# Performance work log

Hardware: AMD Instinct MI355X
Metric: run time of the kernel (lower is better)

Reference implementation:

```python
import jax, jax.numpy as jnp
import numpy as np


def setup_inputs() -> dict:
    key = jax.random.key(0)
    k1, k2, k3 = jax.random.split(key, 3)
    B, S, H, E = 4, 4096, 7168, 256
    return {
        "hidden_states": jax.random.normal(k1, (B, S, H), dtype=jnp.float32),
        "gate_weight": jax.random.normal(k2, (E, H), dtype=jnp.float32) * (H ** -0.5),
        "bias": jax.random.normal(k3, (E,), dtype=jnp.float32) * 0.01,
        "n_group": 8,
        "topk_group": 4,
        "top_k": 8,
    }


def reference(hidden_states, gate_weight, bias, n_group, topk_group, top_k):
    B, S, H = hidden_states.shape
    E = gate_weight.shape[0]
    group_size = E // n_group
    x = hidden_states.reshape(-1, H)  # [T, H]
    logits = jnp.einsum("th,eh->te", x, gate_weight)  # [T, E]
    scores = jax.nn.sigmoid(logits) + bias  # [T, E]
    scores_g = scores.reshape(-1, n_group, group_size)  # [T, G, E/G]
    group_scores = scores_g.max(axis=-1)  # [T, G]
    _, sel_groups = jax.lax.top_k(group_scores, topk_group)  # [T, topk_group]
    # group mask: 1.0 for selected groups (indices are distinct, so sum of one-hots is 0/1)
    group_mask = jax.nn.one_hot(sel_groups, n_group, dtype=scores.dtype).sum(axis=1)  # [T, G]
    masked = (scores_g * group_mask[:, :, None]).reshape(-1, E)  # [T, E]
    weights, indices = jax.lax.top_k(masked, top_k)  # [T, top_k]
    weights = weights / (weights.sum(axis=-1, keepdims=True) + 1e-6)
    return weights.reshape(B, S, -1), indices.reshape(B, S, -1)
```

## Files before the change

### kernel.cpp

```cpp
#include <hip/hip_runtime.h>


#define TTOK 16384
#define EEXP 256
#define HDIM 7168
#define BM 64
#define BK 64
#define NSTEP (HDIM / BK)
#define NTHR 512
#define LDS_BYTES 81920

typedef __attribute__((ext_vector_type(4))) float f32x4;
typedef __attribute__((ext_vector_type(4))) _Float16 h4;
typedef __attribute__((ext_vector_type(8))) _Float16 h8;

__global__ __launch_bounds__(256) void convert_w_kernel(
    const float* __restrict__ W, _Float16* __restrict__ whi,
    _Float16* __restrict__ wlo) {
  int i = blockIdx.x * blockDim.x + threadIdx.x;
  f32x4 v = ((const f32x4*)W)[i];
  h4 hi, lo;
#pragma unroll
  for (int j = 0; j < 4; ++j) {
    float x = v[j];
    _Float16 h = (_Float16)x;
    hi[j] = h;
    lo[j] = (_Float16)((x - (float)h) * 2048.0f);
  }
  *(h4*)(whi + (size_t)i * 4) = hi;
  *(h4*)(wlo + (size_t)i * 4) = lo;
}

__device__ __forceinline__ int swz_idx(int r, int kchunk) {
  return r * 64 + ((kchunk ^ (r & 7)) << 3);
}

__global__ __launch_bounds__(NTHR) void gate_kernel(
    const float* __restrict__ X, const _Float16* __restrict__ Whi,
    const _Float16* __restrict__ Wlo, const float* __restrict__ bias,
    float* __restrict__ outw, float* __restrict__ outi) {
  extern __shared__ char smem[];
  _Float16* Ahi = (_Float16*)smem;
  _Float16* Alo = (_Float16*)(smem + 8192);
  _Float16* Bhi = (_Float16*)(smem + 16384);
  _Float16* Blo = (_Float16*)(smem + 49152);
  float (*scores)[EEXP + 1] = (float (*)[EEXP + 1])smem;

  const int tid = threadIdx.x;
  const int lane = tid & 63;
  const int wid = tid >> 6;
  const int wr = wid >> 2;
  const int wc = wid & 3;

  const int ar = tid >> 3;
  const int aq = tid & 7;
  const long arow_base = (long)(blockIdx.x * BM + ar) * HDIM;

  f32x4 ra0, ra1;
  h8 rbh[4], rbl[4];

  f32x4 acc1[2][4], acc2[2][4];
#pragma unroll
  for (int m = 0; m < 2; ++m)
#pragma unroll
    for (int n = 0; n < 4; ++n) {
      acc1[m][n] = (f32x4){0.f, 0.f, 0.f, 0.f};
      acc2[m][n] = (f32x4){0.f, 0.f, 0.f, 0.f};
    }

  auto LOAD = [&](int k0) {
    ra0 = *(const f32x4*)(X + arow_base + k0 + aq * 4);
    ra1 = *(const f32x4*)(X + arow_base + k0 + (aq + 8) * 4);
#pragma unroll
    for (int i = 0; i < 4; ++i) {
      int c = tid + i * 512;
      int r = c >> 3, cc = c & 7;
      const long off = (long)r * HDIM + k0 + cc * 8;
      rbh[i] = *(const h8*)(Whi + off);
      rbl[i] = *(const h8*)(Wlo + off);
    }
  };

  auto STORE = [&]() {
    h4 h0, l0, h1, l1;
#pragma unroll
    for (int j = 0; j < 4; ++j) {
      float x0 = ra0[j];
      _Float16 hh0 = (_Float16)x0;
      h0[j] = hh0;
      l0[j] = (_Float16)((x0 - (float)hh0) * 2048.0f);
      float x1 = ra1[j];
      _Float16 hh1 = (_Float16)x1;
      h1[j] = hh1;
      l1[j] = (_Float16)((x1 - (float)hh1) * 2048.0f);
    }
    {
      int e0 = ar * 64 + ((((aq >> 1)) ^ (ar & 7)) << 3) + (aq & 1) * 4;
      int q1 = aq + 8;
      int e1 = ar * 64 + ((((q1 >> 1)) ^ (ar & 7)) << 3) + (q1 & 1) * 4;
      *(h4*)(Ahi + e0) = h0;
      *(h4*)(Ahi + e1) = h1;
      *(h4*)(Alo + e0) = l0;
      *(h4*)(Alo + e1) = l1;
    }
#pragma unroll
    for (int i = 0; i < 4; ++i) {
      int c = tid + i * 512;
      int r = c >> 3, cc = c & 7;
      int e = swz_idx(r, cc);
      *(h8*)(Bhi + e) = rbh[i];
      *(h8*)(Blo + e) = rbl[i];
    }
  };

  LOAD(0);
#pragma unroll 1
  for (int kk = 0; kk < NSTEP; ++kk) {
    __syncthreads();
    STORE();
    __syncthreads();
    if (kk + 1 < NSTEP) LOAD((kk + 1) * BK);

#pragma unroll
    for (int s = 0; s < 2; ++s) {
      const int cc = ((s * 32 + (lane >> 4) * 8) >> 3);
      h8 ah[2], al[2];
#pragma unroll
      for (int m = 0; m < 2; ++m) {
        int r = wr * 32 + m * 16 + (lane & 15);
        int e = swz_idx(r, cc);
        ah[m] = *(h8*)(Ahi + e);
        al[m] = *(h8*)(Alo + e);
      }
#pragma unroll
      for (int n = 0; n < 4; ++n) {
        int r = wc * 64 + n * 16 + (lane & 15);
        int e = swz_idx(r, cc);
        h8 bh = *(h8*)(Bhi + e);
        h8 bl = *(h8*)(Blo + e);
#pragma unroll
        for (int m = 0; m < 2; ++m) {
          acc1[m][n] = __builtin_amdgcn_mfma_f32_16x16x32_f16(ah[m], bh, acc1[m][n], 0, 0, 0);
          acc2[m][n] = __builtin_amdgcn_mfma_f32_16x16x32_f16(ah[m], bl, acc2[m][n], 0, 0, 0);
          acc2[m][n] = __builtin_amdgcn_mfma_f32_16x16x32_f16(al[m], bh, acc2[m][n], 0, 0, 0);
        }
      }
    }
  }

  __syncthreads();

#pragma unroll
  for (int m = 0; m < 2; ++m)
#pragma unroll
    for (int n = 0; n < 4; ++n) {
      int e = wc * 64 + n * 16 + (lane & 15);
      float b = bias[e];
      int t0 = wr * 32 + m * 16 + (lane >> 4) * 4;
#pragma unroll
      for (int r = 0; r < 4; ++r) {
        float logit = acc1[m][n][r] + acc2[m][n][r] * (1.0f / 2048.0f);
        scores[t0 + r][e] = 1.0f / (1.0f + expf(-logit)) + b;
      }
    }
  __syncthreads();

  if ((lane & 7) == 0) {
    int t = wid * 8 + (lane >> 3);
    const float* sc = scores[t];

    float gmax[8];
#pragma unroll
    for (int g = 0; g < 8; ++g) {
      float mx = -1e30f;
      for (int j = 0; j < 32; ++j) mx = fmaxf(mx, sc[g * 32 + j]);
      gmax[g] = mx;
    }
    unsigned selmask = 0;
    for (int it = 0; it < 4; ++it) {
      float best = -1e30f;
      int bi = 0;
      for (int g = 0; g < 8; ++g)
        if (!((selmask >> g) & 1) && gmax[g] > best) {
          best = gmax[g];
          bi = g;
        }
      selmask |= 1u << bi;
    }
    float vals[8];
    int idx[8];
#pragma unroll
    for (int j = 0; j < 8; ++j) {
      vals[j] = -1e30f;
      idx[j] = 0;
    }
    for (int e = 0; e < 256; ++e) {
      float v = ((selmask >> (e >> 5)) & 1) ? sc[e] : 0.0f;
      if (v > vals[7]) {
        int p = 7;
        while (p > 0 && v > vals[p - 1]) {
          vals[p] = vals[p - 1];
          idx[p] = idx[p - 1];
          --p;
        }
        vals[p] = v;
        idx[p] = e;
      }
    }
    float ssum = 0.0f;
#pragma unroll
    for (int j = 0; j < 8; ++j) ssum += vals[j];
    float den = ssum + 1e-6f;
    long tg = (long)blockIdx.x * BM + t;
#pragma unroll
    for (int j = 0; j < 8; ++j) {
      outw[tg * 8 + j] = vals[j] / den;
      outi[tg * 8 + j] = (float)idx[j];
    }
  }
}

extern "C" void kernel_launch(void* const* d_in, const int* in_sizes, int n_in,
                              void* d_out, int out_size, void* d_ws, size_t ws_size,
                              hipStream_t stream) {
  const float* X = (const float*)d_in[0];
  const float* W = (const float*)d_in[1];
  const float* bias = (const float*)d_in[2];

  _Float16* whi = (_Float16*)d_ws;
  _Float16* wlo = whi + (size_t)EEXP * HDIM;

  float* outw = (float*)d_out;
  float* outi = outw + (size_t)TTOK * 8;

  hipFuncSetAttribute((const void*)gate_kernel,
                      hipFuncAttributeMaxDynamicSharedMemorySize, LDS_BYTES);

  convert_w_kernel<<<(EEXP * HDIM / 4) / 256, 256, 0, stream>>>(W, whi, wlo);
  gate_kernel<<<TTOK / BM, NTHR, LDS_BYTES, stream>>>(X, whi, wlo, bias, outw, outi);
}
```

Measured before the change: 314.6 us.

## Pre-pack gate weights into MFMA fragment layout and stream B from global to registers

The weight hi/lo fp16 split is now written in MFMA-fragment order, so each wave can load its B operands straight from global memory into registers. B is double-buffered across four k sub-steps, which removes the B staging through LDS. The tile changes to 32 tokens by 256 experts with 256 threads and BK=128. This cuts LDS use and synchronisation work per step and should allow more resident blocks. The trade-off is that twice as many blocks each re-read the whole packed weight from L2, raising L2/MALL traffic, and every k step now depends on global-load latency.

```diff
diff --git a/kernel.cpp b/kernel.cpp
--- a/kernel.cpp
+++ b/kernel.cpp
@@ -4,35 +4,37 @@
 #define TTOK 16384
 #define EEXP 256
 #define HDIM 7168
-#define BM 64
-#define BK 64
+#define BM 32
+#define BK 128
 #define NSTEP (HDIM / BK)
-#define NTHR 512
-#define LDS_BYTES 81920
+#define NTHR 256
+#define NKC (HDIM / 32)
+#define LDS_BYTES 33024
 
 typedef __attribute__((ext_vector_type(4))) float f32x4;
 typedef __attribute__((ext_vector_type(4))) _Float16 h4;
 typedef __attribute__((ext_vector_type(8))) _Float16 h8;
 
-__global__ __launch_bounds__(256) void convert_w_kernel(
-    const float* __restrict__ W, _Float16* __restrict__ whi,
-    _Float16* __restrict__ wlo) {
-  int i = blockIdx.x * blockDim.x + threadIdx.x;
-  f32x4 v = ((const f32x4*)W)[i];
-  h4 hi, lo;
-#pragma unroll
-  for (int j = 0; j < 4; ++j) {
-    float x = v[j];
+__global__ __launch_bounds__(64) void pack_w_kernel(const float* __restrict__ W,
+                                                    _Float16* __restrict__ whi,
+                                                    _Float16* __restrict__ wlo) {
+  const int kc = blockIdx.x;
+  const int eb = blockIdx.y;
+  const int lane = threadIdx.x;
+  const int e = eb * 16 + (lane & 15);
+  const int k0 = kc * 32 + (lane >> 4) * 8;
+  const float* src = W + (size_t)e * HDIM + k0;
+  h8 hi, lo;
+#pragma unroll
+  for (int j = 0; j < 8; ++j) {
+    float x = src[j];
     _Float16 h = (_Float16)x;
     hi[j] = h;
     lo[j] = (_Float16)((x - (float)h) * 2048.0f);
   }
-  *(h4*)(whi + (size_t)i * 4) = hi;
-  *(h4*)(wlo + (size_t)i * 4) = lo;
-}
-
-__device__ __forceinline__ int swz_idx(int r, int kchunk) {
-  return r * 64 + ((kchunk ^ (r & 7)) << 3);
+  const size_t fi = ((size_t)(eb * NKC + kc) * 64 + lane) * 8;
+  *(h8*)(whi + fi) = hi;
+  *(h8*)(wlo + fi) = lo;
 }
 
 __global__ __launch_bounds__(NTHR) void gate_kernel(
@@ -42,22 +44,17 @@
   extern __shared__ char smem[];
   _Float16* Ahi = (_Float16*)smem;
   _Float16* Alo = (_Float16*)(smem + 8192);
-  _Float16* Bhi = (_Float16*)(smem + 16384);
-  _Float16* Blo = (_Float16*)(smem + 49152);
   float (*scores)[EEXP + 1] = (float (*)[EEXP + 1])smem;
 
   const int tid = threadIdx.x;
   const int lane = tid & 63;
   const int wid = tid >> 6;
-  const int wr = wid >> 2;
-  const int wc = wid & 3;
-
-  const int ar = tid >> 3;
-  const int aq = tid & 7;
-  const long arow_base = (long)(blockIdx.x * BM + ar) * HDIM;
-
-  f32x4 ra0, ra1;
-  h8 rbh[4], rbl[4];
+  const int webase = wid * 4;
+  const int tok0 = blockIdx.x * BM;
+
+  f32x4 ra[4];
+  h8 bh0[4], bl0[4];
+  h8 bh1[4], bl1[4];
 
   f32x4 acc1[2][4], acc2[2][4];
 #pragma unroll
@@ -68,105 +65,100 @@
       acc2[m][n] = (f32x4){0.f, 0.f, 0.f, 0.f};
     }
 
-  auto LOAD = [&](int k0) {
-    ra0 = *(const f32x4*)(X + arow_base + k0 + aq * 4);
-    ra1 = *(const f32x4*)(X + arow_base + k0 + (aq + 8) * 4);
+  auto LOADA = [&](int k0) {
 #pragma unroll
     for (int i = 0; i < 4; ++i) {
-      int c = tid + i * 512;
-      int r = c >> 3, cc = c & 7;
-      const long off = (long)r * HDIM + k0 + cc * 8;
-      rbh[i] = *(const h8*)(Whi + off);
-      rbl[i] = *(const h8*)(Wlo + off);
+      const int p = tid + i * 256;
+      ra[i] = *(const f32x4*)(X + (size_t)(tok0 + (p >> 5)) * HDIM + k0 + (p & 31) * 4);
     }
   };
 
-  auto STORE = [&]() {
-    h4 h0, l0, h1, l1;
-#pragma unroll
-    for (int j = 0; j < 4; ++j) {
-      float x0 = ra0[j];
-      _Float16 hh0 = (_Float16)x0;
-      h0[j] = hh0;
-      l0[j] = (_Float16)((x0 - (float)hh0) * 2048.0f);
-      float x1 = ra1[j];
-      _Float16 hh1 = (_Float16)x1;
-      h1[j] = hh1;
-      l1[j] = (_Float16)((x1 - (float)hh1) * 2048.0f);
-    }
-    {
-      int e0 = ar * 64 + ((((aq >> 1)) ^ (ar & 7)) << 3) + (aq & 1) * 4;
-      int q1 = aq + 8;
-      int e1 = ar * 64 + ((((q1 >> 1)) ^ (ar & 7)) << 3) + (q1 & 1) * 4;
-      *(h4*)(Ahi + e0) = h0;
-      *(h4*)(Ahi + e1) = h1;
-      *(h4*)(Alo + e0) = l0;
-      *(h4*)(Alo + e1) = l1;
-    }
+  auto STOREA = [&]() {
 #pragma unroll
     for (int i = 0; i < 4; ++i) {
-      int c = tid + i * 512;
-      int r = c >> 3, cc = c & 7;
-      int e = swz_idx(r, cc);
-      *(h8*)(Bhi + e) = rbh[i];
-      *(h8*)(Blo + e) = rbl[i];
+      const int p = tid + i * 256;
+      const int row = p >> 5, q = p & 31;
+      h4 hi, lo;
+#pragma unroll
+      for (int j = 0; j < 4; ++j) {
+        float x = ra[i][j];
+        _Float16 h = (_Float16)x;
+        hi[j] = h;
+        lo[j] = (_Float16)((x - (float)h) * 2048.0f);
+      }
+      const int ix = row * BK + (((q >> 1) ^ (row & 15)) << 3) + (q & 1) * 4;
+      *(h4*)(Ahi + ix) = hi;
+      *(h4*)(Alo + ix) = lo;
     }
   };
 
-  LOAD(0);
+#define BLOAD(BH, BL, KC)                                              \
+  {                                                                    \
+    const int kc_ = (KC);                                              \
+    _Pragma("unroll") for (int n = 0; n < 4; ++n) {                    \
+      const long fi_ = ((long)(webase + n) * NKC + kc_) * 64 + lane;   \
+      BH[n] = *(const h8*)(Whi + fi_ * 8);                             \
+      BL[n] = *(const h8*)(Wlo + fi_ * 8);                             \
+    }                                                                  \
+  }
+
+#define PHASE(S, BH, BL)                                                        \
+  {                                                                             \
+    h8 ah[2], al[2];                                                            \
+    _Pragma("unroll") for (int m = 0; m < 2; ++m) {                             \
+      const int r_ = m * 16 + (lane & 15);                                      \
+      const int cc_ = (S) * 4 + (lane >> 4);                                    \
+      const int ix_ = r_ * BK + ((cc_ ^ (r_ & 15)) << 3);                       \
+      ah[m] = *(h8*)(Ahi + ix_);                                                \
+      al[m] = *(h8*)(Alo + ix_);                                                \
+    }                                                                           \
+    _Pragma("unroll") for (int n = 0; n < 4; ++n)                               \
+        _Pragma("unroll") for (int m = 0; m < 2; ++m) {                         \
+      acc1[m][n] = __builtin_amdgcn_mfma_f32_16x16x32_f16(ah[m], BH[n], acc1[m][n], 0, 0, 0); \
+      acc2[m][n] = __builtin_amdgcn_mfma_f32_16x16x32_f16(ah[m], BL[n], acc2[m][n], 0, 0, 0); \
+      acc2[m][n] = __builtin_amdgcn_mfma_f32_16x16x32_f16(al[m], BH[n], acc2[m][n], 0, 0, 0); \
+    }                                                                           \
+  }
+
+  LOADA(0);
+  BLOAD(bh0, bl0, 0);
 #pragma unroll 1
   for (int kk = 0; kk < NSTEP; ++kk) {
     __syncthreads();
-    STORE();
+    STOREA();
     __syncthreads();
-    if (kk + 1 < NSTEP) LOAD((kk + 1) * BK);
-
-#pragma unroll
-    for (int s = 0; s < 2; ++s) {
-      const int cc = ((s * 32 + (lane >> 4) * 8) >> 3);
-      h8 ah[2], al[2];
-#pragma unroll
-      for (int m = 0; m < 2; ++m) {
-        int r = wr * 32 + m * 16 + (lane & 15);
-        int e = swz_idx(r, cc);
-        ah[m] = *(h8*)(Ahi + e);
-        al[m] = *(h8*)(Alo + e);
-      }
-#pragma unroll
-      for (int n = 0; n < 4; ++n) {
-        int r = wc * 64 + n * 16 + (lane & 15);
-        int e = swz_idx(r, cc);
-        h8 bh = *(h8*)(Bhi + e);
-        h8 bl = *(h8*)(Blo + e);
-#pragma unroll
-        for (int m = 0; m < 2; ++m) {
-          acc1[m][n] = __builtin_amdgcn_mfma_f32_16x16x32_f16(ah[m], bh, acc1[m][n], 0, 0, 0);
-          acc2[m][n] = __builtin_amdgcn_mfma_f32_16x16x32_f16(ah[m], bl, acc2[m][n], 0, 0, 0);
-          acc2[m][n] = __builtin_amdgcn_mfma_f32_16x16x32_f16(al[m], bh, acc2[m][n], 0, 0, 0);
-        }
-      }
-    }
+    if (kk + 1 < NSTEP) LOADA((kk + 1) * BK);
+    const int kcb = kk * 4;
+    BLOAD(bh1, bl1, kcb + 1);
+    PHASE(0, bh0, bl0);
+    BLOAD(bh0, bl0, kcb + 2);
+    PHASE(1, bh1, bl1);
+    BLOAD(bh1, bl1, kcb + 3);
+    PHASE(2, bh0, bl0);
+    if (kk + 1 < NSTEP) { BLOAD(bh0, bl0, kcb + 4); }
+    PHASE(3, bh1, bl1);
   }
 
   __syncthreads();
 
+  const int ebase = wid * 64;
 #pragma unroll
   for (int m = 0; m < 2; ++m)
 #pragma unroll
     for (int n = 0; n < 4; ++n) {
-      int e = wc * 64 + n * 16 + (lane & 15);
-      float b = bias[e];
-      int t0 = wr * 32 + m * 16 + (lane >> 4) * 4;
+      const int e = ebase + n * 16 + (lane & 15);
+      const float b = bias[e];
+      const int t0 = m * 16 + (lane >> 4) * 4;
 #pragma unroll
       for (int r = 0; r < 4; ++r) {
-        float logit = acc1[m][n][r] + acc2[m][n][r] * (1.0f / 2048.0f);
+        const float logit = acc1[m][n][r] + acc2[m][n][r] * (1.0f / 2048.0f);
         scores[t0 + r][e] = 1.0f / (1.0f + expf(-logit)) + b;
       }
     }
   __syncthreads();
 
   if ((lane & 7) == 0) {
-    int t = wid * 8 + (lane >> 3);
+    const int t = wid * 8 + (lane >> 3);
     const float* sc = scores[t];
 
     float gmax[8];
@@ -210,8 +202,8 @@
     float ssum = 0.0f;
 #pragma unroll
     for (int j = 0; j < 8; ++j) ssum += vals[j];
-    float den = ssum + 1e-6f;
-    long tg = (long)blockIdx.x * BM + t;
+    const float den = ssum + 1e-6f;
+    const long tg = (long)tok0 + t;
 #pragma unroll
     for (int j = 0; j < 8; ++j) {
       outw[tg * 8 + j] = vals[j] / den;
@@ -236,6 +228,6 @@
   hipFuncSetAttribute((const void*)gate_kernel,
                       hipFuncAttributeMaxDynamicSharedMemorySize, LDS_BYTES);
 
-  convert_w_kernel<<<(EEXP * HDIM / 4) / 256, 256, 0, stream>>>(W, whi, wlo);
+  pack_w_kernel<<<dim3(NKC, EEXP / 16), 64, 0, stream>>>(W, whi, wlo);
   gate_kernel<<<TTOK / BM, NTHR, LDS_BYTES, stream>>>(X, whi, wlo, bias, outw, outi);
 }
```

Result: slower. 332.4 us (+5.6%).
